# Kernel tuning notes

Hardware: AMD Instinct MI355X
Metric: run time of the kernel (lower is better)

Reference implementation:

```python
import jax, jax.numpy as jnp
import numpy as np

HID = 128
N_LAYERS = 4
IN_DIM = 2


def _gru_layer(x_seq, W_ih, W_hh, b_ih, b_hh):
    """PyTorch-equivalent single GRU layer.
    x_seq: (T, N, F); W_ih: (3H, F); W_hh: (3H, H); b_ih, b_hh: (3H,)
    Gate order (PyTorch): r, z, n.
    """
    T, N, _ = x_seq.shape
    # precompute input projections for all timesteps: (T, N, 3H)
    gi = jnp.einsum('tnf,gf->tng', x_seq, W_ih) + b_ih

    def step(h, gi_t):
        gh = h @ W_hh.T + b_hh                      # (N, 3H)
        gi_r, gi_z, gi_n = jnp.split(gi_t, 3, axis=-1)
        gh_r, gh_z, gh_n = jnp.split(gh, 3, axis=-1)
        r = jax.nn.sigmoid(gi_r + gh_r)
        z = jax.nn.sigmoid(gi_z + gh_z)
        n = jnp.tanh(gi_n + r * gh_n)
        h_new = (1.0 - z) * n + z * h
        return h_new, h_new

    h0 = jnp.zeros((N, HID), dtype=x_seq.dtype)
    _, out = jax.lax.scan(step, h0, gi)
    return out                                       # (T, N, H)


def setup_inputs() -> dict:
    key = jax.random.key(0)
    ks = jax.random.split(key, 12)
    s = 1.0 / np.sqrt(HID)  # PyTorch GRU init scale
    x = jax.random.normal(ks[0], (512, IN_DIM, 1024), dtype=jnp.float32)
    W_ih0 = jax.random.uniform(ks[1], (3 * HID, IN_DIM), minval=-s, maxval=s)
    W_ih_rest = jax.random.uniform(ks[2], (N_LAYERS - 1, 3 * HID, HID), minval=-s, maxval=s)
    W_hh = jax.random.uniform(ks[3], (N_LAYERS, 3 * HID, HID), minval=-s, maxval=s)
    b_ih = jax.random.uniform(ks[4], (N_LAYERS, 3 * HID), minval=-s, maxval=s)
    b_hh = jax.random.uniform(ks[5], (N_LAYERS, 3 * HID), minval=-s, maxval=s)
    fc1_w = jax.random.uniform(ks[6], (HID, HID), minval=-s, maxval=s)
    fc1_b = jax.random.uniform(ks[7], (HID,), minval=-s, maxval=s)
    fc2_w = jax.random.uniform(ks[8], (3, HID), minval=-s, maxval=s)
    fc2_b = jax.random.uniform(ks[9], (3,), minval=-s, maxval=s)
    return {"x": x, "W_ih0": W_ih0, "W_ih_rest": W_ih_rest, "W_hh": W_hh,
            "b_ih": b_ih, "b_hh": b_hh, "fc1_w": fc1_w, "fc1_b": fc1_b,
            "fc2_w": fc2_w, "fc2_b": fc2_b}


def reference(x, W_ih0, W_ih_rest, W_hh, b_ih, b_hh, fc1_w, fc1_b, fc2_w, fc2_b):
    # x: (B, 2, S) -> transpose(1,2) -> (B, S, 2); GRU (batch_first=False)
    # treats axis0 as time T=B, axis1 as batch N=S.
    h = jnp.transpose(x, (0, 2, 1))                  # (T, N, 2)
    h = _gru_layer(h, W_ih0, W_hh[0], b_ih[0], b_hh[0])
    for l in range(1, N_LAYERS):
        h = _gru_layer(h, W_ih_rest[l - 1], W_hh[l], b_ih[l], b_hh[l])
    # out[:, -1, :] -> last lane along the GRU batch axis: (T, H)
    last = h[:, -1, :]
    hidden = jax.nn.relu(last @ fc1_w.T + fc1_b)
    return hidden @ fc2_w.T + fc2_b                  # (B, 3)
```

## Files before the change

### kernel.cpp

```cpp
#include <hip/hip_runtime.h>
#include <math.h>

#define T_SEQ  512
#define HID    128
#define G3     384
#define NL     4
#define CHUNK  8
#define NCHUNK (T_SEQ / CHUNK)

#define GI_TOT   (NL * T_SEQ * G3)
#define SEQ_TOT  (NL * T_SEQ * HID)
#define FLAG_OFF (GI_TOT + SEQ_TOT)

__device__ __forceinline__ float fsig(float x) {
    float e = __expf(-x);
    return 1.0f / (1.0f + e);
}
__device__ __forceinline__ float ftanh(float x) {
    float ax = fabsf(x);
    float e = __expf(-2.0f * ax);
    float t = (1.0f - e) / (1.0f + e);
    return copysignf(t, x);
}


__global__ void init_flags(int* fl) {
    int i = threadIdx.x;
    if (i < 8) fl[i * 16] = (i == 0) ? NCHUNK : 0;
}

__global__ void gi0_kernel(const float* __restrict__ x, const float* __restrict__ Wih0,
                           const float* __restrict__ bih, float* __restrict__ gi) {
    int t = blockIdx.x;
    int g = threadIdx.x;
    float x0 = x[t * 2048 + 1023];
    float x1 = x[t * 2048 + 1024 + 1023];
    gi[t * G3 + g] = bih[g] + Wih0[g * 2 + 0] * x0 + Wih0[g * 2 + 1] * x1;
}

#define PK_DOT16(S0, S1, W2, H2)                    \
    _Pragma("unroll")                               \
    for (int pc = 0; pc < 16; pc += 2) {            \
        S0 += W2[pc]     * H2[pc];                  \
        S1 += W2[pc + 1] * H2[pc + 1];              \
    }

__global__ __launch_bounds__(256, 1) void pipe_kernel(float* __restrict__ ws,
                                                      const float* __restrict__ WihR,
                                                      const float* __restrict__ bih,
                                                      const float* __restrict__ Whh,
                                                      const float* __restrict__ bhh) {
    __shared__ float smem[2688];
    float* h_s  = smem;
    float* ps   = smem + 128;
    float* aux  = smem + 1664;

    int bid = blockIdx.x;
    int tid = threadIdx.x;
    int q   = tid >> 6;
    int rg  = tid & 63;
    int row0 = rg * 6;
    int* fl = (int*)(ws + FLAG_OFF);
    bool is_rec = (bid & 1) == 0;
    int  l      = is_rec ? (bid >> 1) : ((bid + 1) >> 1);

    if (is_rec) {
        const float* W   = Whh + (size_t)l * G3 * HID;
        const float* gi  = ws + (size_t)l * T_SEQ * G3;
        float* seq_o     = ws + GI_TOT + (size_t)l * T_SEQ * HID;
        int* in_flag     = &fl[l * 16];
        int* out_flag    = &fl[(4 + l) * 16];

        float w[6][32];
        const float* wbase = W + q * 32;
#pragma unroll
        for (int i = 0; i < 6; i++) {
            const float4* wr = reinterpret_cast<const float4*>(wbase + (size_t)(row0 + i) * HID);
#pragma unroll
            for (int c = 0; c < 8; c++) {
                float4 v = wr[c];
                w[i][c * 4 + 0] = v.x; w[i][c * 4 + 1] = v.y;
                w[i][c * 4 + 2] = v.z; w[i][c * 4 + 3] = v.w;
            }
        }

        float hprev = 0.f, br = 0.f, bz = 0.f, bn = 0.f;
        float g_r[CHUNK], g_z[CHUNK], g_n[CHUNK];
        if (tid < HID) {
            h_s[tid] = 0.0f;
            const float* bb = bhh + (size_t)l * G3;
            br = bb[tid]; bz = bb[HID + tid]; bn = bb[2 * HID + tid];
        }
        __syncthreads();

        for (int c = 0; c < NCHUNK; c++) {
            if (tid == 0) {
                while (__hip_atomic_fetch_add(in_flag, 0, __ATOMIC_RELAXED, __HIP_MEMORY_SCOPE_AGENT) < c + 1)
                    __builtin_amdgcn_s_sleep(2);
            }
            __syncthreads();
            int t0 = c * CHUNK;
            if (tid < HID) {
                const float* gp = gi + (size_t)t0 * G3 + tid;
#pragma unroll
                for (int s = 0; s < CHUNK; s++) {
                    g_r[s] = gp[s * G3];
                    g_z[s] = gp[s * G3 + HID];
                    g_n[s] = gp[s * G3 + 2 * HID];
                }
            }
#pragma unroll
            for (int s = 0; s < CHUNK; s++) {
                const float4* h4 = reinterpret_cast<const float4*>(h_s + q * 32);
                float4 hv[8];
#pragma unroll
                for (int cc = 0; cc < 8; cc++) hv[cc] = h4[cc];
                const float2* h2 = reinterpret_cast<const float2*>(hv);
                float acc[6];
#pragma unroll
                for (int i = 0; i < 6; i++) {
                    const float2* w2 = reinterpret_cast<const float2*>(w[i]);
                    float2 s0 = {0.f, 0.f}, s1 = {0.f, 0.f};
                    PK_DOT16(s0, s1, w2, h2);
                    acc[i] = (s0.x + s0.y) + (s1.x + s1.y);
                }
#pragma unroll
                for (int i = 0; i < 6; i += 2) {
                    float2 p; p.x = acc[i]; p.y = acc[i + 1];
                    *reinterpret_cast<float2*>(&ps[q * G3 + row0 + i]) = p;
                }
                __syncthreads();
                if (tid < HID) {
                    int j = tid;
                    float ghr = (ps[j]         + ps[G3 + j])         + (ps[2*G3 + j]         + ps[3*G3 + j]);
                    float ghz = (ps[HID + j]   + ps[G3 + HID + j])   + (ps[2*G3 + HID + j]   + ps[3*G3 + HID + j]);
                    float ghn = (ps[2*HID + j] + ps[G3 + 2*HID + j]) + (ps[2*G3 + 2*HID + j] + ps[3*G3 + 2*HID + j]);
                    float r = fsig(g_r[s] + ghr + br);
                    float z = fsig(g_z[s] + ghz + bz);
                    float n = ftanh(g_n[s] + r * (ghn + bn));
                    float hn = (1.0f - z) * n + z * hprev;
                    hprev = hn;
                    h_s[j] = hn;
                    aux[s * HID + j] = hn;
                }
                __syncthreads();
            }
            {
                float4 v = *reinterpret_cast<const float4*>(&aux[tid * 4]);
                *reinterpret_cast<float4*>(&seq_o[(size_t)t0 * HID + tid * 4]) = v;
            }
            __syncthreads();
            if (tid == 0)
                __hip_atomic_store(out_flag, c + 1, __ATOMIC_RELEASE, __HIP_MEMORY_SCOPE_AGENT);
        }
    } else {
        const float* W   = WihR + (size_t)(l - 1) * G3 * HID;
        const float* seq_in = ws + GI_TOT + (size_t)(l - 1) * T_SEQ * HID;
        float* gi_o      = ws + (size_t)l * T_SEQ * G3;
        int* in_flag     = &fl[(4 + (l - 1)) * 16];
        int* out_flag    = &fl[l * 16];

        float w[6][32];
        const float* wbase = W + q * 32;
#pragma unroll
        for (int i = 0; i < 6; i++) {
            const float4* wr = reinterpret_cast<const float4*>(wbase + (size_t)(row0 + i) * HID);
#pragma unroll
            for (int c = 0; c < 8; c++) {
                float4 v = wr[c];
                w[i][c * 4 + 0] = v.x; w[i][c * 4 + 1] = v.y;
                w[i][c * 4 + 2] = v.z; w[i][c * 4 + 3] = v.w;
            }
        }
        float br = 0.f, bz = 0.f, bn = 0.f;
        float o_r[CHUNK], o_z[CHUNK], o_n[CHUNK];
        if (tid < HID) {
            const float* bb = bih + (size_t)l * G3;
            br = bb[tid]; bz = bb[HID + tid]; bn = bb[2 * HID + tid];
        }

        for (int c = 0; c < NCHUNK; c++) {
            if (tid == 0) {
                while (__hip_atomic_fetch_add(in_flag, 0, __ATOMIC_RELAXED, __HIP_MEMORY_SCOPE_AGENT) < c + 1)
                    __builtin_amdgcn_s_sleep(2);
            }
            __syncthreads();
            int t0 = c * CHUNK;
            {
                float4 v = *reinterpret_cast<const float4*>(&seq_in[(size_t)t0 * HID + tid * 4]);
                *reinterpret_cast<float4*>(&aux[tid * 4]) = v;
            }
            __syncthreads();
#pragma unroll
            for (int s = 0; s < CHUNK; s++) {
                const float4* h4 = reinterpret_cast<const float4*>(aux + s * HID + q * 32);
                float4 hv[8];
#pragma unroll
                for (int cc = 0; cc < 8; cc++) hv[cc] = h4[cc];
                const float2* h2 = reinterpret_cast<const float2*>(hv);
                float acc[6];
#pragma unroll
                for (int i = 0; i < 6; i++) {
                    const float2* w2 = reinterpret_cast<const float2*>(w[i]);
                    float2 s0 = {0.f, 0.f}, s1 = {0.f, 0.f};
                    PK_DOT16(s0, s1, w2, h2);
                    acc[i] = (s0.x + s0.y) + (s1.x + s1.y);
                }
#pragma unroll
                for (int i = 0; i < 6; i += 2) {
                    float2 p; p.x = acc[i]; p.y = acc[i + 1];
                    *reinterpret_cast<float2*>(&ps[q * G3 + row0 + i]) = p;
                }
                __syncthreads();
                if (tid < HID) {
                    int j = tid;
                    o_r[s] = (ps[j]         + ps[G3 + j])         + (ps[2*G3 + j]         + ps[3*G3 + j]);
                    o_z[s] = (ps[HID + j]   + ps[G3 + HID + j])   + (ps[2*G3 + HID + j]   + ps[3*G3 + HID + j]);
                    o_n[s] = (ps[2*HID + j] + ps[G3 + 2*HID + j]) + (ps[2*G3 + 2*HID + j] + ps[3*G3 + 2*HID + j]);
                }
                __syncthreads();
            }
            if (tid < HID) {
                int j = tid;
                float* gp = gi_o + (size_t)t0 * G3 + j;
#pragma unroll
                for (int s = 0; s < CHUNK; s++) {
                    gp[s * G3]           = o_r[s] + br;
                    gp[s * G3 + HID]     = o_z[s] + bz;
                    gp[s * G3 + 2 * HID] = o_n[s] + bn;
                }
            }
            __syncthreads();
            if (tid == 0)
                __hip_atomic_store(out_flag, c + 1, __ATOMIC_RELEASE, __HIP_MEMORY_SCOPE_AGENT);
        }
    }
}

__global__ void fc_kernel(const float* __restrict__ seq, const float* __restrict__ fc1w,
                          const float* __restrict__ fc1b, const float* __restrict__ fc2w,
                          const float* __restrict__ fc2b, float* __restrict__ out) {
    __shared__ float h3[HID];
    __shared__ float hid[HID];
    int t = blockIdx.x;
    int i = threadIdx.x;
    h3[i] = seq[t * HID + i];
    __syncthreads();
    const float4* w4 = reinterpret_cast<const float4*>(fc1w + i * HID);
    const float4* h4 = reinterpret_cast<const float4*>(h3);
    float a0 = 0.f, a1 = 0.f, a2 = 0.f, a3 = 0.f;
#pragma unroll
    for (int k = 0; k < 32; k += 4) {
        float4 w0 = w4[k], w1 = w4[k + 1], w2 = w4[k + 2], w3 = w4[k + 3];
        float4 h0 = h4[k], h1 = h4[k + 1], h2 = h4[k + 2], h3v = h4[k + 3];
        a0 += w0.x * h0.x + w0.y * h0.y + w0.z * h0.z + w0.w * h0.w;
        a1 += w1.x * h1.x + w1.y * h1.y + w1.z * h1.z + w1.w * h1.w;
        a2 += w2.x * h2.x + w2.y * h2.y + w2.z * h2.z + w2.w * h2.w;
        a3 += w3.x * h3v.x + w3.y * h3v.y + w3.z * h3v.z + w3.w * h3v.w;
    }
    float v = fc1b[i] + ((a0 + a1) + (a2 + a3));
    hid[i] = v > 0.0f ? v : 0.0f;
    __syncthreads();
    if (i < 3) {
        const float* w = fc2w + i * HID;
        float s = 0.f;
#pragma unroll
        for (int k = 0; k < HID; k++) s += w[k] * hid[k];
        out[t * 3 + i] = fc2b[i] + s;
    }
}

extern "C" void kernel_launch(void* const* d_in, const int* in_sizes, int n_in,
                              void* d_out, int out_size, void* d_ws, size_t ws_size,
                              hipStream_t stream) {
    const float* x     = (const float*)d_in[0];
    const float* Wih0  = (const float*)d_in[1];
    const float* WihR  = (const float*)d_in[2];
    const float* Whh   = (const float*)d_in[3];
    const float* bih   = (const float*)d_in[4];
    const float* bhh   = (const float*)d_in[5];
    const float* fc1w  = (const float*)d_in[6];
    const float* fc1b  = (const float*)d_in[7];
    const float* fc2w  = (const float*)d_in[8];
    const float* fc2b  = (const float*)d_in[9];
    float* out = (float*)d_out;
    float* ws  = (float*)d_ws;

    int*   flags = (int*)(ws + FLAG_OFF);
    float* gi0   = ws;
    float* seq3  = ws + GI_TOT + (size_t)3 * T_SEQ * HID;

    init_flags<<<1, 64, 0, stream>>>(flags);
    gi0_kernel<<<T_SEQ, G3, 0, stream>>>(x, Wih0, bih, gi0);
    pipe_kernel<<<7, 256, 0, stream>>>(ws, WihR, bih, Whh, bhh);
    fc_kernel<<<T_SEQ, HID, 0, stream>>>(seq3, fc1w, fc1b, fc2w, fc2b, out);
}
```

Before: 427.7 us.

## Broadcast hidden state via readlane and double-buffer partials to drop a barrier

In the recurrent blocks, each wave now rebuilds its 32-element slice of the hidden state from its own lanes with readlane broadcasts instead of reading it from shared memory. The partial-sum buffer is double-buffered by timestep parity, which removes the second barrier per step. The input-projection blocks now write all 8 timesteps' partials before a single barrier and spread the reduction and gi store across all 256 threads. This shortens the serial per-step critical path at the cost of more scalar readlane instructions and redundant gate computation in each wave.

Result: faster. 394.0 us (-7.9%).

```diff
diff --git a/kernel.cpp b/kernel.cpp
--- a/kernel.cpp
+++ b/kernel.cpp
@@ -21,6 +21,9 @@
     float e = __expf(-2.0f * ax);
     float t = (1.0f - e) / (1.0f + e);
     return copysignf(t, x);
+}
+__device__ __forceinline__ float rdlane(float v, int k) {
+    return __uint_as_float(__builtin_amdgcn_readlane(__float_as_uint(v), k));
 }
 
 
@@ -38,28 +41,18 @@
     gi[t * G3 + g] = bih[g] + Wih0[g * 2 + 0] * x0 + Wih0[g * 2 + 1] * x1;
 }
 
-#define PK_DOT16(S0, S1, W2, H2)                    \
-    _Pragma("unroll")                               \
-    for (int pc = 0; pc < 16; pc += 2) {            \
-        S0 += W2[pc]     * H2[pc];                  \
-        S1 += W2[pc + 1] * H2[pc + 1];              \
-    }
-
 __global__ __launch_bounds__(256, 1) void pipe_kernel(float* __restrict__ ws,
                                                       const float* __restrict__ WihR,
                                                       const float* __restrict__ bih,
                                                       const float* __restrict__ Whh,
                                                       const float* __restrict__ bhh) {
-    __shared__ float smem[2688];
-    float* h_s  = smem;
-    float* ps   = smem + 128;
-    float* aux  = smem + 1664;
-
-    int bid = blockIdx.x;
-    int tid = threadIdx.x;
-    int q   = tid >> 6;
-    int rg  = tid & 63;
-    int row0 = rg * 6;
+    __shared__ float smem[12288];
+
+    int bid  = blockIdx.x;
+    int tid  = threadIdx.x;
+    int lane = tid & 63;
+    int q    = tid >> 6;
+    int row0 = lane * 6;
     int* fl = (int*)(ws + FLAG_OFF);
     bool is_rec = (bid & 1) == 0;
     int  l      = is_rec ? (bid >> 1) : ((bid + 1) >> 1);
@@ -68,6 +61,7 @@
         const float* W   = Whh + (size_t)l * G3 * HID;
         const float* gi  = ws + (size_t)l * T_SEQ * G3;
         float* seq_o     = ws + GI_TOT + (size_t)l * T_SEQ * HID;
+        float* aux       = smem + 3072;
         int* in_flag     = &fl[l * 16];
         int* out_flag    = &fl[(4 + l) * 16];
 
@@ -84,14 +78,18 @@
             }
         }
 
-        float hprev = 0.f, br = 0.f, bz = 0.f, bn = 0.f;
+        int  m  = lane & 31;
+        bool p2 = (lane < 32);
+        int  j  = q * 32 + m;
+        const float* bb = bhh + (size_t)l * G3;
+        float br = 0.f, bz = 0.f, bn = 0.f;
+        if (p2) { br = bb[j]; bz = bb[HID + j]; bn = bb[2 * HID + j]; }
+
+        float hs[32];
+#pragma unroll
+        for (int k = 0; k < 32; k++) hs[k] = 0.f;
+        float hprev = 0.f;
         float g_r[CHUNK], g_z[CHUNK], g_n[CHUNK];
-        if (tid < HID) {
-            h_s[tid] = 0.0f;
-            const float* bb = bhh + (size_t)l * G3;
-            br = bb[tid]; bz = bb[HID + tid]; bn = bb[2 * HID + tid];
-        }
-        __syncthreads();
 
         for (int c = 0; c < NCHUNK; c++) {
             if (tid == 0) {
@@ -100,8 +98,8 @@
             }
             __syncthreads();
             int t0 = c * CHUNK;
-            if (tid < HID) {
-                const float* gp = gi + (size_t)t0 * G3 + tid;
+            if (p2) {
+                const float* gp = gi + (size_t)t0 * G3 + j;
 #pragma unroll
                 for (int s = 0; s < CHUNK; s++) {
                     g_r[s] = gp[s * G3];
@@ -111,40 +109,44 @@
             }
 #pragma unroll
             for (int s = 0; s < CHUNK; s++) {
-                const float4* h4 = reinterpret_cast<const float4*>(h_s + q * 32);
-                float4 hv[8];
-#pragma unroll
-                for (int cc = 0; cc < 8; cc++) hv[cc] = h4[cc];
-                const float2* h2 = reinterpret_cast<const float2*>(hv);
+                int t = t0 + s;
+                float* psb = smem + (t & 1) * 1536;
                 float acc[6];
 #pragma unroll
                 for (int i = 0; i < 6; i++) {
-                    const float2* w2 = reinterpret_cast<const float2*>(w[i]);
-                    float2 s0 = {0.f, 0.f}, s1 = {0.f, 0.f};
-                    PK_DOT16(s0, s1, w2, h2);
-                    acc[i] = (s0.x + s0.y) + (s1.x + s1.y);
+                    float a0 = 0.f, a1 = 0.f, a2 = 0.f, a3 = 0.f;
+#pragma unroll
+                    for (int k = 0; k < 32; k += 4) {
+                        a0 += w[i][k]     * hs[k];
+                        a1 += w[i][k + 1] * hs[k + 1];
+                        a2 += w[i][k + 2] * hs[k + 2];
+                        a3 += w[i][k + 3] * hs[k + 3];
+                    }
+                    acc[i] = (a0 + a1) + (a2 + a3);
                 }
 #pragma unroll
                 for (int i = 0; i < 6; i += 2) {
                     float2 p; p.x = acc[i]; p.y = acc[i + 1];
-                    *reinterpret_cast<float2*>(&ps[q * G3 + row0 + i]) = p;
+                    *reinterpret_cast<float2*>(&psb[q * G3 + row0 + i]) = p;
                 }
                 __syncthreads();
-                if (tid < HID) {
-                    int j = tid;
-                    float ghr = (ps[j]         + ps[G3 + j])         + (ps[2*G3 + j]         + ps[3*G3 + j]);
-                    float ghz = (ps[HID + j]   + ps[G3 + HID + j])   + (ps[2*G3 + HID + j]   + ps[3*G3 + HID + j]);
-                    float ghn = (ps[2*HID + j] + ps[G3 + 2*HID + j]) + (ps[2*G3 + 2*HID + j] + ps[3*G3 + 2*HID + j]);
+                float hn_bc = 0.f;
+                if (p2) {
+                    float ghr = (psb[j]         + psb[G3 + j])         + (psb[2*G3 + j]         + psb[3*G3 + j]);
+                    float ghz = (psb[HID + j]   + psb[G3 + HID + j])   + (psb[2*G3 + HID + j]   + psb[3*G3 + HID + j]);
+                    float ghn = (psb[2*HID + j] + psb[G3 + 2*HID + j]) + (psb[2*G3 + 2*HID + j] + psb[3*G3 + 2*HID + j]);
                     float r = fsig(g_r[s] + ghr + br);
                     float z = fsig(g_z[s] + ghz + bz);
                     float n = ftanh(g_n[s] + r * (ghn + bn));
                     float hn = (1.0f - z) * n + z * hprev;
                     hprev = hn;
-                    h_s[j] = hn;
                     aux[s * HID + j] = hn;
-                }
-                __syncthreads();
-            }
+                    hn_bc = hn;
+                }
+#pragma unroll
+                for (int k = 0; k < 32; k++) hs[k] = rdlane(hn_bc, k);
+            }
+            __syncthreads();
             {
                 float4 v = *reinterpret_cast<const float4*>(&aux[tid * 4]);
                 *reinterpret_cast<float4*>(&seq_o[(size_t)t0 * HID + tid * 4]) = v;
@@ -172,11 +174,15 @@
                 w[i][c * 4 + 2] = v.z; w[i][c * 4 + 3] = v.w;
             }
         }
-        float br = 0.f, bz = 0.f, bn = 0.f;
-        float o_r[CHUNK], o_z[CHUNK], o_n[CHUNK];
-        if (tid < HID) {
-            const float* bb = bih + (size_t)l * G3;
-            br = bb[tid]; bz = bb[HID + tid]; bn = bb[2 * HID + tid];
+        int m  = lane & 31;
+        int m2 = tid & 31;
+        int s2 = tid >> 5;
+        const float* bb = bih + (size_t)l * G3;
+        float br4[4], bz4[4], bn4[4];
+#pragma unroll
+        for (int u = 0; u < 4; u++) {
+            int jj = u * 32 + m2;
+            br4[u] = bb[jj]; bz4[u] = bb[HID + jj]; bn4[u] = bb[2 * HID + jj];
         }
 
         for (int c = 0; c < NCHUNK; c++) {
@@ -186,49 +192,49 @@
             }
             __syncthreads();
             int t0 = c * CHUNK;
+            float vseq[CHUNK];
             {
-                float4 v = *reinterpret_cast<const float4*>(&seq_in[(size_t)t0 * HID + tid * 4]);
-                *reinterpret_cast<float4*>(&aux[tid * 4]) = v;
-            }
-            __syncthreads();
+                const float* sp = seq_in + (size_t)t0 * HID + q * 32 + m;
+#pragma unroll
+                for (int s = 0; s < CHUNK; s++) vseq[s] = sp[s * HID];
+            }
 #pragma unroll
             for (int s = 0; s < CHUNK; s++) {
-                const float4* h4 = reinterpret_cast<const float4*>(aux + s * HID + q * 32);
-                float4 hv[8];
-#pragma unroll
-                for (int cc = 0; cc < 8; cc++) hv[cc] = h4[cc];
-                const float2* h2 = reinterpret_cast<const float2*>(hv);
+                float xs[32];
+#pragma unroll
+                for (int k = 0; k < 32; k++) xs[k] = rdlane(vseq[s], k);
                 float acc[6];
 #pragma unroll
                 for (int i = 0; i < 6; i++) {
-                    const float2* w2 = reinterpret_cast<const float2*>(w[i]);
-                    float2 s0 = {0.f, 0.f}, s1 = {0.f, 0.f};
-                    PK_DOT16(s0, s1, w2, h2);
-                    acc[i] = (s0.x + s0.y) + (s1.x + s1.y);
-                }
+                    float a0 = 0.f, a1 = 0.f, a2 = 0.f, a3 = 0.f;
+#pragma unroll
+                    for (int k = 0; k < 32; k += 4) {
+                        a0 += w[i][k]     * xs[k];
+                        a1 += w[i][k + 1] * xs[k + 1];
+                        a2 += w[i][k + 2] * xs[k + 2];
+                        a3 += w[i][k + 3] * xs[k + 3];
+                    }
+                    acc[i] = (a0 + a1) + (a2 + a3);
+                }
+                float* pp = smem + s * 1536;
 #pragma unroll
                 for (int i = 0; i < 6; i += 2) {
                     float2 p; p.x = acc[i]; p.y = acc[i + 1];
-                    *reinterpret_cast<float2*>(&ps[q * G3 + row0 + i]) = p;
-                }
-                __syncthreads();
-                if (tid < HID) {
-                    int j = tid;
-                    o_r[s] = (ps[j]         + ps[G3 + j])         + (ps[2*G3 + j]         + ps[3*G3 + j]);
-                    o_z[s] = (ps[HID + j]   + ps[G3 + HID + j])   + (ps[2*G3 + HID + j]   + ps[3*G3 + HID + j]);
-                    o_n[s] = (ps[2*HID + j] + ps[G3 + 2*HID + j]) + (ps[2*G3 + 2*HID + j] + ps[3*G3 + 2*HID + j]);
-                }
-                __syncthreads();
-            }
-            if (tid < HID) {
-                int j = tid;
-                float* gp = gi_o + (size_t)t0 * G3 + j;
-#pragma unroll
-                for (int s = 0; s < CHUNK; s++) {
-                    gp[s * G3]           = o_r[s] + br;
-                    gp[s * G3 + HID]     = o_z[s] + bz;
-                    gp[s * G3 + 2 * HID] = o_n[s] + bn;
-                }
+                    *reinterpret_cast<float2*>(&pp[q * G3 + row0 + i]) = p;
+                }
+            }
+            __syncthreads();
+#pragma unroll
+            for (int u = 0; u < 4; u++) {
+                int jj = u * 32 + m2;
+                const float* pp = smem + s2 * 1536;
+                float vr = (pp[jj]         + pp[G3 + jj])         + (pp[2*G3 + jj]         + pp[3*G3 + jj]);
+                float vz = (pp[HID + jj]   + pp[G3 + HID + jj])   + (pp[2*G3 + HID + jj]   + pp[3*G3 + HID + jj]);
+                float vn = (pp[2*HID + jj] + pp[G3 + 2*HID + jj]) + (pp[2*G3 + 2*HID + jj] + pp[3*G3 + 2*HID + jj]);
+                float* gp = gi_o + (size_t)(t0 + s2) * G3;
+                gp[jj]           = vr + br4[u];
+                gp[HID + jj]     = vz + bz4[u];
+                gp[2 * HID + jj] = vn + bn4[u];
             }
             __syncthreads();
             if (tid == 0)
```
